# Performance work log

Hardware: AMD Instinct MI355X
Metric: run time of the kernel (lower is better)

Reference implementation:

```python
import jax, jax.numpy as jnp
import numpy as np

DIM = 512
QK_DIM = 128
HIDDEN = 1024


def setup_inputs() -> dict:
    key = jax.random.key(0)
    ks = jax.random.split(key, 8)
    b, n = 4, 4096
    x = jax.random.normal(ks[0], (b, n, DIM), dtype=jnp.float32)
    # nn.Linear(dim, hidden*2)
    w_hidden = jax.random.normal(ks[1], (DIM, 2 * HIDDEN), dtype=jnp.float32) / np.sqrt(DIM)
    b_hidden = jnp.zeros((2 * HIDDEN,), dtype=jnp.float32)
    # nn.Linear(dim, qk_dim, bias=False)
    w_qk = jax.random.normal(ks[2], (DIM, QK_DIM), dtype=jnp.float32) / np.sqrt(DIM)
    # OffsetScale params (gamma init 1, beta init 0; randomize slightly for a nontrivial test)
    q_gamma = 1.0 + 0.02 * jax.random.normal(ks[3], (QK_DIM,), dtype=jnp.float32)
    q_beta = 0.02 * jax.random.normal(ks[4], (QK_DIM,), dtype=jnp.float32)
    k_gamma = 1.0 + 0.02 * jax.random.normal(ks[5], (QK_DIM,), dtype=jnp.float32)
    k_beta = 0.02 * jax.random.normal(ks[6], (QK_DIM,), dtype=jnp.float32)
    # nn.Linear(hidden, dim)
    w_out = jax.random.normal(ks[7], (HIDDEN, DIM), dtype=jnp.float32) / np.sqrt(HIDDEN)
    b_out = jnp.zeros((DIM,), dtype=jnp.float32)
    return {
        "x": x,
        "w_hidden": w_hidden, "b_hidden": b_hidden,
        "w_qk": w_qk,
        "q_gamma": q_gamma, "q_beta": q_beta,
        "k_gamma": k_gamma, "k_beta": k_beta,
        "w_out": w_out, "b_out": b_out,
    }


def reference(x, w_hidden, b_hidden, w_qk, q_gamma, q_beta, k_gamma, k_beta, w_out, b_out):
    scale = QK_DIM ** -0.5
    # to_hidden -> chunk into v, gate (NOTE: source applies no activation here)
    hid = jnp.einsum('bnd,dh->bnh', x, w_hidden) + b_hidden  # [b, n, 2*hidden]
    v, gate = jnp.split(hid, 2, axis=-1)                     # each [b, n, hidden]
    qk = jnp.einsum('bnd,de->bne', x, w_qk)                  # [b, n, qk_dim]
    q = qk * q_gamma + q_beta
    k = qk * k_gamma + k_beta
    sim = jnp.einsum('bid,bjd->bij', q, k) * scale           # [b, n, n]
    attn = jnp.square(jax.nn.relu(sim))                      # ReLU^2, no softmax
    out = jnp.einsum('bij,bjh->bih', attn, v)                # [b, n, hidden]
    out = out * gate
    out = jnp.einsum('bnh,hd->bnd', out, w_out) + b_out      # [b, n, dim]
    return out + x  # add_residual=True
```

## Files before the change

### kernel.cpp

```cpp
#include <hip/hip_runtime.h>
#include <hip/hip_bf16.h>

typedef __attribute__((ext_vector_type(8))) short bf16x8;
typedef __attribute__((ext_vector_type(4))) float f32x4;
typedef unsigned short u16;

__device__ __forceinline__ u16 f2b(float f) {
  __hip_bfloat16 h = __float2bfloat16(f);
  return __builtin_bit_cast(unsigned short, h);
}
__device__ __forceinline__ float b2f(u16 u) {
  __hip_bfloat16 h = __builtin_bit_cast(__hip_bfloat16, u);
  return __bfloat162float(h);
}

#define BAR() __builtin_amdgcn_s_barrier()
#define LGKM0() do { asm volatile("s_waitcnt lgkmcnt(0)" ::: "memory"); __builtin_amdgcn_sched_barrier(0); } while (0)
#define VMCNT4() asm volatile("s_waitcnt vmcnt(4)" ::: "memory")
#define VMCNT0() asm volatile("s_waitcnt vmcnt(0)" ::: "memory")

#define EPI_HID 0
#define EPI_QK 1
#define EPI_ATTN 2
#define EPI_PV 3
#define EPI_OUT 4

__device__ __forceinline__ void stage_tile(char* sbase, const char* gbase, int ld_bytes, int tid) {
#pragma unroll
  for (int i = 0; i < 4; ++i) {
    int o = (i * 256 + tid) * 16;
    int row = o >> 7;
    int cb = o & 127;
    int scb = cb ^ ((row & 7) << 4);
    const char* src = gbase + (long)row * ld_bytes + scb;
    __builtin_amdgcn_global_load_lds((const __attribute__((address_space(1))) void*)src,
                                     (__attribute__((address_space(3))) void*)(sbase + o),
                                     16, 0, 0);
  }
}

template <int EPI>
__global__ __launch_bounds__(256, 2) void gemm_tn(
    const char* Ab, const char* Bb, long sAbat, long sBbat,
    int lda_b, int ldb_b, int nkt,
    u16* o0, u16* o1,
    const float* a0, const float* a1, const float* a2, const float* a3,
    float* fout, const float* xres) {
  __shared__ __align__(16) char lds[32768];
  char* sA = lds;
  char* sB = lds + 16384;
  const int tid = threadIdx.x;
  const int lane = tid & 63;
  const int wave = tid >> 6;
  const int wm = wave >> 1, wn = wave & 1;
  const int l16 = lane & 15, lq = lane >> 4;
  const int bat = blockIdx.z;
  const int row0 = blockIdx.y * 128;
  const int col0 = blockIdx.x * 128;

  const char* Abase = Ab + (long)bat * sAbat + (long)row0 * lda_b;
  const char* Bbase = Bb + (long)bat * sBbat + (long)col0 * ldb_b;

  f32x4 acc[4][4];
#pragma unroll
  for (int i = 0; i < 4; ++i)
#pragma unroll
    for (int j = 0; j < 4; ++j) acc[i][j] = (f32x4){0.f, 0.f, 0.f, 0.f};

  for (int kt = 0; kt < nkt; ++kt) {
    stage_tile(sA, Abase + (long)kt * 128, lda_b, tid);
    stage_tile(sB, Bbase + (long)kt * 128, ldb_b, tid);
    __syncthreads();
#pragma unroll
    for (int kk = 0; kk < 2; ++kk) {
      bf16x8 af[4], bfr[4];
#pragma unroll
      for (int mf = 0; mf < 4; ++mf) {
        int r = wm * 64 + mf * 16 + l16;
        int kb = kk * 64 + lq * 16;
        af[mf] = *(const bf16x8*)(sA + r * 128 + (kb ^ ((r & 7) << 4)));
      }
#pragma unroll
      for (int nf = 0; nf < 4; ++nf) {
        int r = wn * 64 + nf * 16 + l16;
        int kb = kk * 64 + lq * 16;
        bfr[nf] = *(const bf16x8*)(sB + r * 128 + (kb ^ ((r & 7) << 4)));
      }
#pragma unroll
      for (int mf = 0; mf < 4; ++mf)
#pragma unroll
        for (int nf = 0; nf < 4; ++nf)
          acc[mf][nf] = __builtin_amdgcn_mfma_f32_16x16x32_bf16(af[mf], bfr[nf], acc[mf][nf], 0, 0, 0);
    }
    __syncthreads();
  }

#pragma unroll
  for (int mf = 0; mf < 4; ++mf) {
#pragma unroll
    for (int nf = 0; nf < 4; ++nf) {
      const int row = row0 + wm * 64 + mf * 16 + lq * 4;
      const int col = col0 + wn * 64 + nf * 16 + l16;
      f32x4 v = acc[mf][nf];
      if constexpr (EPI == EPI_QK) {
        float qg = a0[col], qbt = a1[col], kg = a2[col], kbt = a3[col];
#pragma unroll
        for (int i = 0; i < 4; ++i) {
          float t = v[i];
          o0[(size_t)(row + i) * 128 + col] = f2b(t * qg + qbt);
          o1[(size_t)(row + i) * 128 + col] = f2b(t * kg + kbt);
        }
      } else if constexpr (EPI == EPI_OUT) {
        float bias = a0[col];
#pragma unroll
        for (int i = 0; i < 4; ++i)
          fout[(size_t)(row + i) * 512 + col] = v[i] + bias + xres[(size_t)(row + i) * 512 + col];
      }
    }
  }
}

__device__ __forceinline__ void stage_half(char* sbase, const char* gbase, long ld, int tid) {
#pragma unroll
  for (int i = 0; i < 2; ++i) {
    int o = (i * 512 + tid) * 16;
    int row = o >> 7;
    int cb = o & 127;
    int scb = cb ^ ((row & 7) << 4);
    const char* src = gbase + (long)row * ld + scb;
    __builtin_amdgcn_global_load_lds((const __attribute__((address_space(1))) void*)src,
                                     (__attribute__((address_space(3))) void*)(sbase + o),
                                     16, 0, 0);
  }
}

template <int EPI>
__global__ __launch_bounds__(512, 2) void gemm256(
    const char* Ab, const char* Bb, long sAbat, long sBbat,
    long lda, long ldb, int nkt, int nx,
    u16* o0, u16* o1,
    const float* a0, float* fout, const float* xres) {
  extern __shared__ __align__(16) char lds[];
  const int tid = threadIdx.x;
  const int lane = tid & 63;
  const int wave = tid >> 6;
  const int wm = wave >> 2;
  const int wn = wave & 3;
  const int l16 = lane & 15, lq = lane >> 4;
  const int bat = blockIdx.y;

  const int nwg = gridDim.x;
  const int qq = nwg >> 3;
  const int fid = blockIdx.x;
  const int swz = (fid & 7) * qq + (fid >> 3);
  const int row0 = (swz / nx) * 256;
  const int col0 = (swz % nx) * 256;

  const char* gA = Ab + (long)bat * sAbat + (long)row0 * lda;
  const char* gB = Bb + (long)bat * sBbat + (long)col0 * ldb;

  f32x4 acc[8][4];
#pragma unroll
  for (int i = 0; i < 8; ++i)
#pragma unroll
    for (int j = 0; j < 4; ++j) acc[i][j] = (f32x4){0.f, 0.f, 0.f, 0.f};

  const int kmask = (l16 & 7) << 4;

  stage_half(lds + 32768, gB, ldb, tid);
  stage_half(lds + 32768 + 16384, gB + 128 * ldb, ldb, tid);
  stage_half(lds, gA, lda, tid);
  stage_half(lds + 16384, gA + 128 * lda, lda, tid);
  if (nkt > 1) {
    stage_half(lds + 65536 + 32768, gB + 128, ldb, tid);
    stage_half(lds + 65536 + 32768 + 16384, gB + 128 * ldb + 128, ldb, tid);
    VMCNT4();
  } else {
    VMCNT0();
  }
  BAR();

  bf16x8 af[4][2], bfr[4][2];

  for (int t = 0; t < nkt; ++t) {
    const char* buf = lds + (t & 1) * 65536;
    const char* myA = buf + wm * 16384;
    const char* myB = buf + 32768 + (wn >> 1) * 16384;
    const int rB = (wn & 1) * 64;
    char* stA = lds + ((t + 1) & 1) * 65536;
    char* stB = lds + (t & 1) * 65536 + 32768;
    const bool sA_ok = (t + 1) < nkt;
    const bool sB_ok = (t + 2) < nkt;

#pragma unroll
    for (int nf = 0; nf < 2; ++nf) {
      int r = rB + nf * 16 + l16;
#pragma unroll
      for (int kh = 0; kh < 2; ++kh)
        bfr[nf][kh] = *(const bf16x8*)(myB + r * 128 + ((kh * 64 + lq * 16) ^ kmask));
    }
#pragma unroll
    for (int mf = 0; mf < 4; ++mf) {
      int r = mf * 16 + l16;
#pragma unroll
      for (int kh = 0; kh < 2; ++kh)
        af[mf][kh] = *(const bf16x8*)(myA + r * 128 + ((kh * 64 + lq * 16) ^ kmask));
    }
    if (sA_ok) stage_half(stA, gA + (long)(t + 1) * 128, lda, tid);
    BAR();
    LGKM0();
    __builtin_amdgcn_s_setprio(1);
#pragma unroll
    for (int mf = 0; mf < 4; ++mf)
#pragma unroll
      for (int nf = 0; nf < 2; ++nf)
#pragma unroll
        for (int kh = 0; kh < 2; ++kh)
          acc[mf][nf] = __builtin_amdgcn_mfma_f32_16x16x32_bf16(af[mf][kh], bfr[nf][kh], acc[mf][nf], 0, 0, 0);
    __builtin_amdgcn_s_setprio(0);
    BAR();

#pragma unroll
    for (int nf = 2; nf < 4; ++nf) {
      int r = rB + nf * 16 + l16;
#pragma unroll
      for (int kh = 0; kh < 2; ++kh)
        bfr[nf][kh] = *(const bf16x8*)(myB + r * 128 + ((kh * 64 + lq * 16) ^ kmask));
    }
    if (sA_ok) stage_half(stA + 16384, gA + 128 * lda + (long)(t + 1) * 128, lda, tid);
    BAR();
    LGKM0();
    __builtin_amdgcn_s_setprio(1);
#pragma unroll
    for (int mf = 0; mf < 4; ++mf)
#pragma unroll
      for (int nf = 2; nf < 4; ++nf)
#pragma unroll
        for (int kh = 0; kh < 2; ++kh)
          acc[mf][nf] = __builtin_amdgcn_mfma_f32_16x16x32_bf16(af[mf][kh], bfr[nf][kh], acc[mf][nf], 0, 0, 0);
    __builtin_amdgcn_s_setprio(0);
    BAR();

#pragma unroll
    for (int mf = 0; mf < 4; ++mf) {
      int r = 64 + mf * 16 + l16;
#pragma unroll
      for (int kh = 0; kh < 2; ++kh)
        af[mf][kh] = *(const bf16x8*)(myA + r * 128 + ((kh * 64 + lq * 16) ^ kmask));
    }
    if (sB_ok) stage_half(stB, gB + (long)(t + 2) * 128, ldb, tid);
    BAR();
    LGKM0();
    __builtin_amdgcn_s_setprio(1);
#pragma unroll
    for (int mf = 0; mf < 4; ++mf)
#pragma unroll
      for (int nf = 2; nf < 4; ++nf)
#pragma unroll
        for (int kh = 0; kh < 2; ++kh)
          acc[4 + mf][nf] = __builtin_amdgcn_mfma_f32_16x16x32_bf16(af[mf][kh], bfr[nf][kh], acc[4 + mf][nf], 0, 0, 0);
    __builtin_amdgcn_s_setprio(0);
    BAR();

    if (sB_ok) stage_half(stB + 16384, gB + 128 * ldb + (long)(t + 2) * 128, ldb, tid);
    __builtin_amdgcn_s_setprio(1);
#pragma unroll
    for (int mf = 0; mf < 4; ++mf)
#pragma unroll
      for (int nf = 0; nf < 2; ++nf)
#pragma unroll
        for (int kh = 0; kh < 2; ++kh)
          acc[4 + mf][nf] = __builtin_amdgcn_mfma_f32_16x16x32_bf16(af[mf][kh], bfr[nf][kh], acc[4 + mf][nf], 0, 0, 0);
    __builtin_amdgcn_s_setprio(0);
    if (sB_ok) { VMCNT4(); } else if (sA_ok) { VMCNT0(); }
    BAR();
  }

#pragma unroll
  for (int mi = 0; mi < 8; ++mi) {
#pragma unroll
    for (int ni = 0; ni < 4; ++ni) {
      const int row = row0 + wm * 128 + mi * 16 + lq * 4;
      const int col = col0 + wn * 64 + ni * 16 + l16;
      f32x4 v = acc[mi][ni];
      if constexpr (EPI == EPI_HID) {
        float bias = a0[col];
        u16* dst = (col < 1024) ? (o0 + (size_t)col * 16384 + row)
                                : (o1 + (size_t)(col - 1024) * 16384 + row);
        *(ushort4*)dst = make_ushort4(f2b(v.x + bias), f2b(v.y + bias), f2b(v.z + bias), f2b(v.w + bias));
      } else if constexpr (EPI == EPI_ATTN) {
        const float scale = 0.088388347648318447f;
        u16* dst = o0 + (size_t)bat * 4096 * 4096;
#pragma unroll
        for (int i = 0; i < 4; ++i) {
          float t = v[i] * scale;
          t = t > 0.f ? t * t : 0.f;
          dst[(size_t)(row + i) * 4096 + col] = f2b(t);
        }
      } else if constexpr (EPI == EPI_PV) {
        const u16* gt = o1 + (size_t)col * 16384 + (size_t)bat * 4096 + row;
        ushort4 g = *(const ushort4*)gt;
        u16* dst = o0 + (size_t)bat * 4096 * 1024;
        dst[(size_t)(row + 0) * 1024 + col] = f2b(v.x * b2f(g.x));
        dst[(size_t)(row + 1) * 1024 + col] = f2b(v.y * b2f(g.y));
        dst[(size_t)(row + 2) * 1024 + col] = f2b(v.z * b2f(g.z));
        dst[(size_t)(row + 3) * 1024 + col] = f2b(v.w * b2f(g.w));
      }
    }
  }
}

__global__ void conv_b(const float* in, u16* out, int n) {
  int i = (blockIdx.x * blockDim.x + threadIdx.x) * 4;
  if (i >= n) return;
  float4 f = *(const float4*)(in + i);
  *(ushort4*)(out + i) = make_ushort4(f2b(f.x), f2b(f.y), f2b(f.z), f2b(f.w));
}

__global__ void transpose_b(const float* in, u16* out, int R, int C) {
  int o = blockIdx.x * blockDim.x + threadIdx.x;
  if (o >= R * C) return;
  int c = o / R, r = o - c * R;
  out[o] = f2b(in[(size_t)r * C + c]);
}

extern "C" void kernel_launch(void* const* d_in, const int* in_sizes, int n_in,
                              void* d_out, int out_size, void* d_ws, size_t ws_size,
                              hipStream_t stream) {
  const float* x = (const float*)d_in[0];
  const float* w_hidden = (const float*)d_in[1];
  const float* b_hidden = (const float*)d_in[2];
  const float* w_qk = (const float*)d_in[3];
  const float* q_gamma = (const float*)d_in[4];
  const float* q_beta = (const float*)d_in[5];
  const float* k_gamma = (const float*)d_in[6];
  const float* k_beta = (const float*)d_in[7];
  const float* w_out = (const float*)d_in[8];
  const float* b_out = (const float*)d_in[9];
  float* out = (float*)d_out;

  char* ws = (char*)d_ws;
  size_t off = 0;
  auto alloc = [&](size_t bytes) { char* p = ws + off; off += (bytes + 255) & ~255ull; return p; };
  u16* xb     = (u16*)alloc(16384ull * 512 * 2);
  u16* wh_t   = (u16*)alloc(2048ull * 512 * 2);
  u16* wqk_t  = (u16*)alloc(128ull * 512 * 2);
  u16* wout_t = (u16*)alloc(512ull * 1024 * 2);
  u16* v_t    = (u16*)alloc(1024ull * 16384 * 2);
  u16* g_t    = (u16*)alloc(1024ull * 16384 * 2);
  u16* qb_a   = (u16*)alloc(16384ull * 128 * 2);
  u16* kb_a   = (u16*)alloc(16384ull * 128 * 2);
  u16* attnb  = (u16*)alloc(4ull * 4096 * 4096 * 2);
  u16* out1b  = (u16*)alloc(16384ull * 1024 * 2);

  (void)hipFuncSetAttribute((const void*)gemm256<EPI_HID>, hipFuncAttributeMaxDynamicSharedMemorySize, 131072);
  (void)hipFuncSetAttribute((const void*)gemm256<EPI_ATTN>, hipFuncAttributeMaxDynamicSharedMemorySize, 131072);
  (void)hipFuncSetAttribute((const void*)gemm256<EPI_PV>, hipFuncAttributeMaxDynamicSharedMemorySize, 131072);

  conv_b<<<(16384 * 512 / 4 + 255) / 256, 256, 0, stream>>>(x, xb, 16384 * 512);
  transpose_b<<<(512 * 2048 + 255) / 256, 256, 0, stream>>>(w_hidden, wh_t, 512, 2048);
  transpose_b<<<(512 * 128 + 255) / 256, 256, 0, stream>>>(w_qk, wqk_t, 512, 128);
  transpose_b<<<(1024 * 512 + 255) / 256, 256, 0, stream>>>(w_out, wout_t, 1024, 512);

  gemm256<EPI_HID><<<dim3(512, 1), 512, 131072, stream>>>(
      (const char*)xb, (const char*)wh_t, 0, 0, 1024, 1024, 8, 8,
      v_t, g_t, b_hidden, nullptr, nullptr);
  gemm_tn<EPI_QK><<<dim3(1, 128, 1), 256, 0, stream>>>(
      (const char*)xb, (const char*)wqk_t, 0, 0, 1024, 1024, 8,
      qb_a, kb_a, q_gamma, q_beta, k_gamma, k_beta, nullptr, nullptr);
  gemm256<EPI_ATTN><<<dim3(256, 4), 512, 131072, stream>>>(
      (const char*)qb_a, (const char*)kb_a, 4096ll * 256, 4096ll * 256, 256, 256, 2, 16,
      attnb, nullptr, nullptr, nullptr, nullptr);
  gemm256<EPI_PV><<<dim3(64, 4), 512, 131072, stream>>>(
      (const char*)attnb, (const char*)v_t, 4096ll * 8192, 8192, 8192, 32768, 64, 4,
      out1b, g_t, nullptr, nullptr, nullptr);
  gemm_tn<EPI_OUT><<<dim3(4, 128, 1), 256, 0, stream>>>(
      (const char*)out1b, (const char*)wout_t, 0, 0, 2048, 2048, 16,
      nullptr, nullptr, b_out, nullptr, nullptr, nullptr, out, x);
}
```

Before: 320.6 us.

## Split GEMM main loop by K half instead of N half for fragment reuse

Reorganizes the four-phase inner loop of the 256x256 bf16 MFMA GEMM so each phase covers one K-half (64 bytes) across all four N fragments, instead of both K-halves across two N fragments. B fragments for each K-half are held in separate register sets (bfr0/bfr1) and reused across both M halves, while A fragments are reloaded per K-half. This changes register pressure (A fragments halved, B kept) and adds an extra A LDS read phase plus a barrier and lgkmcnt wait before the last MFMA block. The aim is a different balance of LDS traffic against registers, possibly improving occupancy or scheduling.

```diff
diff --git a/kernel.cpp b/kernel.cpp
--- a/kernel.cpp
+++ b/kernel.cpp
@@ -166,6 +166,8 @@
     for (int j = 0; j < 4; ++j) acc[i][j] = (f32x4){0.f, 0.f, 0.f, 0.f};
 
   const int kmask = (l16 & 7) << 4;
+  const int kb0 = (lq * 16) ^ kmask;
+  const int kb1 = (64 + lq * 16) ^ kmask;
 
   stage_half(lds + 32768, gB, ldb, tid);
   stage_half(lds + 32768 + 16384, gB + 128 * ldb, ldb, tid);
@@ -180,7 +182,7 @@
   }
   BAR();
 
-  bf16x8 af[4][2], bfr[4][2];
+  bf16x8 af[4], bfr0[4], bfr1[4];
 
   for (int t = 0; t < nkt; ++t) {
     const char* buf = lds + (t & 1) * 65536;
@@ -193,19 +195,11 @@
     const bool sB_ok = (t + 2) < nkt;
 
 #pragma unroll
-    for (int nf = 0; nf < 2; ++nf) {
-      int r = rB + nf * 16 + l16;
-#pragma unroll
-      for (int kh = 0; kh < 2; ++kh)
-        bfr[nf][kh] = *(const bf16x8*)(myB + r * 128 + ((kh * 64 + lq * 16) ^ kmask));
-    }
-#pragma unroll
-    for (int mf = 0; mf < 4; ++mf) {
-      int r = mf * 16 + l16;
-#pragma unroll
-      for (int kh = 0; kh < 2; ++kh)
-        af[mf][kh] = *(const bf16x8*)(myA + r * 128 + ((kh * 64 + lq * 16) ^ kmask));
-    }
+    for (int nf = 0; nf < 4; ++nf)
+      bfr0[nf] = *(const bf16x8*)(myB + (rB + nf * 16 + l16) * 128 + kb0);
+#pragma unroll
+    for (int mf = 0; mf < 4; ++mf)
+      af[mf] = *(const bf16x8*)(myA + (mf * 16 + l16) * 128 + kb0);
     if (sA_ok) stage_half(stA, gA + (long)(t + 1) * 128, lda, tid);
     BAR();
     LGKM0();
@@ -213,20 +207,17 @@
 #pragma unroll
     for (int mf = 0; mf < 4; ++mf)
 #pragma unroll
-      for (int nf = 0; nf < 2; ++nf)
-#pragma unroll
-        for (int kh = 0; kh < 2; ++kh)
-          acc[mf][nf] = __builtin_amdgcn_mfma_f32_16x16x32_bf16(af[mf][kh], bfr[nf][kh], acc[mf][nf], 0, 0, 0);
+      for (int nf = 0; nf < 4; ++nf)
+        acc[mf][nf] = __builtin_amdgcn_mfma_f32_16x16x32_bf16(af[mf], bfr0[nf], acc[mf][nf], 0, 0, 0);
     __builtin_amdgcn_s_setprio(0);
     BAR();
 
 #pragma unroll
-    for (int nf = 2; nf < 4; ++nf) {
-      int r = rB + nf * 16 + l16;
-#pragma unroll
-      for (int kh = 0; kh < 2; ++kh)
-        bfr[nf][kh] = *(const bf16x8*)(myB + r * 128 + ((kh * 64 + lq * 16) ^ kmask));
-    }
+    for (int nf = 0; nf < 4; ++nf)
+      bfr1[nf] = *(const bf16x8*)(myB + (rB + nf * 16 + l16) * 128 + kb1);
+#pragma unroll
+    for (int mf = 0; mf < 4; ++mf)
+      af[mf] = *(const bf16x8*)(myA + (mf * 16 + l16) * 128 + kb1);
     if (sA_ok) stage_half(stA + 16384, gA + 128 * lda + (long)(t + 1) * 128, lda, tid);
     BAR();
     LGKM0();
@@ -234,20 +225,14 @@
 #pragma unroll
     for (int mf = 0; mf < 4; ++mf)
 #pragma unroll
-      for (int nf = 2; nf < 4; ++nf)
-#pragma unroll
-        for (int kh = 0; kh < 2; ++kh)
-          acc[mf][nf] = __builtin_amdgcn_mfma_f32_16x16x32_bf16(af[mf][kh], bfr[nf][kh], acc[mf][nf], 0, 0, 0);
+      for (int nf = 0; nf < 4; ++nf)
+        acc[mf][nf] = __builtin_amdgcn_mfma_f32_16x16x32_bf16(af[mf], bfr1[nf], acc[mf][nf], 0, 0, 0);
     __builtin_amdgcn_s_setprio(0);
     BAR();
 
 #pragma unroll
-    for (int mf = 0; mf < 4; ++mf) {
-      int r = 64 + mf * 16 + l16;
-#pragma unroll
-      for (int kh = 0; kh < 2; ++kh)
-        af[mf][kh] = *(const bf16x8*)(myA + r * 128 + ((kh * 64 + lq * 16) ^ kmask));
-    }
+    for (int mf = 0; mf < 4; ++mf)
+      af[mf] = *(const bf16x8*)(myA + (64 + mf * 16 + l16) * 128 + kb0);
     if (sB_ok) stage_half(stB, gB + (long)(t + 2) * 128, ldb, tid);
     BAR();
     LGKM0();
@@ -255,22 +240,23 @@
 #pragma unroll
     for (int mf = 0; mf < 4; ++mf)
 #pragma unroll
-      for (int nf = 2; nf < 4; ++nf)
-#pragma unroll
-        for (int kh = 0; kh < 2; ++kh)
-          acc[4 + mf][nf] = __builtin_amdgcn_mfma_f32_16x16x32_bf16(af[mf][kh], bfr[nf][kh], acc[4 + mf][nf], 0, 0, 0);
+      for (int nf = 0; nf < 4; ++nf)
+        acc[4 + mf][nf] = __builtin_amdgcn_mfma_f32_16x16x32_bf16(af[mf], bfr0[nf], acc[4 + mf][nf], 0, 0, 0);
     __builtin_amdgcn_s_setprio(0);
     BAR();
 
+#pragma unroll
+    for (int mf = 0; mf < 4; ++mf)
+      af[mf] = *(const bf16x8*)(myA + (64 + mf * 16 + l16) * 128 + kb1);
     if (sB_ok) stage_half(stB + 16384, gB + 128 * ldb + (long)(t + 2) * 128, ldb, tid);
+    BAR();
+    LGKM0();
     __builtin_amdgcn_s_setprio(1);
 #pragma unroll
     for (int mf = 0; mf < 4; ++mf)
 #pragma unroll
-      for (int nf = 0; nf < 2; ++nf)
-#pragma unroll
-        for (int kh = 0; kh < 2; ++kh)
-          acc[4 + mf][nf] = __builtin_amdgcn_mfma_f32_16x16x32_bf16(af[mf][kh], bfr[nf][kh], acc[4 + mf][nf], 0, 0, 0);
+      for (int nf = 0; nf < 4; ++nf)
+        acc[4 + mf][nf] = __builtin_amdgcn_mfma_f32_16x16x32_bf16(af[mf], bfr1[nf], acc[4 + mf][nf], 0, 0, 0);
     __builtin_amdgcn_s_setprio(0);
     if (sB_ok) { VMCNT4(); } else if (sA_ok) { VMCNT0(); }
     BAR();
```

Result: no change. 321.8 us (+0.4%).
